# Kernel optimization log

Measured on AMD Instinct MI355X. Metric: run time of the kernel, lower is better.

The kernel has to match this reference:

```python
import jax, jax.numpy as jnp
import numpy as np


def _cxcywh_to_xyxy(b):
    cx, cy, w, h = b[..., 0], b[..., 1], b[..., 2], b[..., 3]
    return jnp.stack([cx - 0.5 * w, cy - 0.5 * h, cx + 0.5 * w, cy + 0.5 * h], axis=-1)


def _generalized_box_iou(a, b):
    # a: [M,4] xyxy, b: [N,4] xyxy -> [M,N] GIoU matrix (DETR box_ops semantics)
    area_a = (a[:, 2] - a[:, 0]) * (a[:, 3] - a[:, 1])  # [M]
    area_b = (b[:, 2] - b[:, 0]) * (b[:, 3] - b[:, 1])  # [N]
    lt = jnp.maximum(a[:, None, :2], b[None, :, :2])    # [M,N,2]
    rb = jnp.minimum(a[:, None, 2:], b[None, :, 2:])
    wh = jnp.clip(rb - lt, 0.0)
    inter = wh[..., 0] * wh[..., 1]                     # [M,N]
    union = area_a[:, None] + area_b[None, :] - inter
    iou = inter / union
    lt_c = jnp.minimum(a[:, None, :2], b[None, :, :2])
    rb_c = jnp.maximum(a[:, None, 2:], b[None, :, 2:])
    wh_c = jnp.clip(rb_c - lt_c, 0.0)
    area_c = wh_c[..., 0] * wh_c[..., 1]
    return iou - (area_c - union) / area_c


def setup_inputs() -> dict:
    key = jax.random.key(0)
    k1, k2, k3 = jax.random.split(key, 3)
    B, T, N = 8, 64, 8
    # predicted boxes in cxcywh, all components in (0,1) -> positive w,h (valid)
    pred_boxes = jax.random.uniform(k1, (B, T, N, 4), dtype=jnp.float32)
    # target boxes directly in valid xyxy (code path uses them unconverted)
    centers = jax.random.uniform(k2, (B, T, N, 2), dtype=jnp.float32) * 0.8 + 0.1
    half_wh = (jax.random.uniform(k3, (B, T, N, 2), dtype=jnp.float32) * 0.2 + 0.02) * 0.5
    bboxes = jnp.concatenate([centers - half_wh, centers + half_wh], axis=-1)
    bboxes_mask = jnp.ones((B, T), dtype=bool)
    return {"pred_boxes": pred_boxes, "bboxes": bboxes, "bboxes_mask": bboxes_mask}


def reference(pred_boxes, bboxes, bboxes_mask):
    B, T, N, _ = pred_boxes.shape
    M = B * T * N
    # per-box validity (mask is per-frame, broadcast to boxes), as weights
    v = jnp.broadcast_to(bboxes_mask[:, :, None], (B, T, N)).reshape(M).astype(pred_boxes.dtype)
    src = _cxcywh_to_xyxy(pred_boxes.reshape(M, 4))   # [M,4]
    tgt = bboxes.reshape(M, 4)                        # [M,4]
    G = _generalized_box_iou(tgt, src)                # [M,M] rows=targets, cols=preds
    # argmax matching over valid prediction columns
    g_match = jnp.where(v[None, :] > 0, G, -jnp.inf)
    idx = jnp.argmax(g_match, axis=1)                 # [M]
    matched = src[idx]                                # [M,4]
    matched_gious = G[:, idx]                         # [M,M] (faithful to original)
    w = v[:, None] * v[idx][None, :]                  # validity weights
    loss_giou = 1.0 - jnp.sum(matched_gious * w) / jnp.sum(w)
    loss_bbox = jnp.sum(jnp.abs(matched - tgt) * v[:, None]) / (4.0 * jnp.sum(v))
    return loss_giou, loss_bbox
```

## Files before the change

### kernel.cpp

```cpp
#include <hip/hip_runtime.h>
#include <cmath>

#define WAVE 64
#define TPB  256
#define RPW  4
#define SJ   8
#define FTPB 1024
#define MMAX 4096

__device__ __forceinline__ float fastrcp(float x) { return __builtin_amdgcn_rcpf(x); }

__device__ __forceinline__ float giou_f(float a0, float a1, float a2, float a3, float areaA,
                                        float b0, float b1, float b2, float b3, float areaB) {
    float ltx = fmaxf(a0, b0), lty = fmaxf(a1, b1);
    float rbx = fminf(a2, b2), rby = fminf(a3, b3);
    float w = fmaxf(rbx - ltx, 0.0f), h = fmaxf(rby - lty, 0.0f);
    float inter = w * h;
    float uni = areaA + areaB - inter;
    float cx1 = fminf(a0, b0), cy1 = fminf(a1, b1);
    float cx2 = fmaxf(a2, b2), cy2 = fmaxf(a3, b3);
    float areaC = (cx2 - cx1) * (cy2 - cy1);
    return inter * fastrcp(uni) - (areaC - uni) * fastrcp(areaC);
}

__device__ __forceinline__ unsigned sortable_u32(float f) {
    unsigned b = __float_as_uint(f);
    return (b & 0x80000000u) ? ~b : (b | 0x80000000u);
}

__device__ __forceinline__ int mask_mode(const void* maskp) {
    const unsigned char* mb = (const unsigned char*)maskp;
    unsigned char b0 = mb[0], b1 = mb[1];
    if (b0 != 0 && b1 != 0) return 0;
    if (b0 != 0) return 1;
    return 2;
}
__device__ __forceinline__ float mask_v(const void* maskp, int t, int mode) {
    if (mode == 0) return ((const unsigned char*)maskp)[t] ? 1.0f : 0.0f;
    if (mode == 1) return ((const int*)maskp)[t] ? 1.0f : 0.0f;
    return (((const float*)maskp)[t] != 0.0f) ? 1.0f : 0.0f;
}
__device__ __forceinline__ int midx(int m, int nsh, int N) {
    return (nsh >= 0) ? (m >> nsh) : (m / N);
}

__global__ __launch_bounds__(TPB) void pass_kernel(
        const float4* __restrict__ pred, const float4* __restrict__ tgt,
        const void* __restrict__ maskp, int M, int nsh, int N,
        unsigned long long* __restrict__ keypart, float* __restrict__ colpart,
        int rowBlocks) {
    const int mode  = mask_mode(maskp);
    const int chunk = M / SJ;
    const int lane  = threadIdx.x & (WAVE - 1);
    const int warp  = threadIdx.x >> 6;

    if ((int)blockIdx.x < rowBlocks) {
        int wid = blockIdx.x * (TPB / WAVE) + warp;
        int rowgrp = wid / SJ, c = wid % SJ;
        int i0 = rowgrp * RPW;
        if (i0 >= M) return;
        int jbeg = c * chunk, jend = jbeg + chunk;

        float a0[RPW], a1[RPW], a2[RPW], a3[RPW], aA[RPW], best[RPW];
        int bidx[RPW];
#pragma unroll
        for (int r = 0; r < RPW; ++r) {
            float4 t = tgt[i0 + r];
            a0[r] = t.x; a1[r] = t.y; a2[r] = t.z; a3[r] = t.w;
            aA[r] = (t.z - t.x) * (t.w - t.y);
            best[r] = -INFINITY; bidx[r] = 0;
        }

#pragma unroll 4
        for (int j = jbeg + lane; j < jend; j += WAVE) {
            float4 p = pred[j];
            float sx1 = p.x - 0.5f * p.z, sy1 = p.y - 0.5f * p.w;
            float sx2 = p.x + 0.5f * p.z, sy2 = p.y + 0.5f * p.w;
            float aB = (sx2 - sx1) * (sy2 - sy1);
            float vj = mask_v(maskp, midx(j, nsh, N), mode);
            bool mv = vj > 0.0f;
#pragma unroll
            for (int r = 0; r < RPW; ++r) {
                float g = giou_f(a0[r], a1[r], a2[r], a3[r], aA[r], sx1, sy1, sx2, sy2, aB);
                float val = mv ? g : -INFINITY;
                if (val > best[r]) { best[r] = val; bidx[r] = j; }
            }
        }

#pragma unroll
        for (int r = 0; r < RPW; ++r) {
            unsigned long long key = ((unsigned long long)sortable_u32(best[r]) << 32)
                                   | (unsigned)(~bidx[r]);
            for (int off = 32; off >= 1; off >>= 1) {
                unsigned long long ok = __shfl_xor(key, off);
                key = (ok > key) ? ok : key;
            }
            if (lane == 0) keypart[(size_t)c * M + (i0 + r)] = key;
        }
    } else {
        int wid = (blockIdx.x - rowBlocks) * (TPB / WAVE) + warp;
        int colgrp = wid / SJ, c = wid % SJ;
        int j0 = colgrp * RPW;
        if (j0 >= M) return;
        int ibeg = c * chunk, iend = ibeg + chunk;

        float b0[RPW], b1[RPW], b2[RPW], b3[RPW], aB[RPW], acc[RPW];
#pragma unroll
        for (int r = 0; r < RPW; ++r) {
            float4 p = pred[j0 + r];
            b0[r] = p.x - 0.5f * p.z; b1[r] = p.y - 0.5f * p.w;
            b2[r] = p.x + 0.5f * p.z; b3[r] = p.y + 0.5f * p.w;
            aB[r] = (b2[r] - b0[r]) * (b3[r] - b1[r]);
            acc[r] = 0.0f;
        }

#pragma unroll 4
        for (int i = ibeg + lane; i < iend; i += WAVE) {
            float4 t = tgt[i];
            float aA = (t.z - t.x) * (t.w - t.y);
            float vi = mask_v(maskp, midx(i, nsh, N), mode);
#pragma unroll
            for (int r = 0; r < RPW; ++r) {
                float g = giou_f(t.x, t.y, t.z, t.w, aA, b0[r], b1[r], b2[r], b3[r], aB[r]);
                acc[r] += vi * g;
            }
        }

#pragma unroll
        for (int r = 0; r < RPW; ++r) {
            for (int off = 32; off >= 1; off >>= 1) acc[r] += __shfl_xor(acc[r], off);
            if (lane == 0) colpart[(size_t)c * M + (j0 + r)] = acc[r];
        }
    }
}

__device__ __forceinline__ double wave_sum_d(double x) {
    for (int off = 32; off >= 1; off >>= 1) x += __shfl_xor(x, off);
    return x;
}

__global__ __launch_bounds__(FTPB) void finalize_kernel(
        const float4* __restrict__ pred, const float4* __restrict__ tgt,
        const void* __restrict__ maskp, int M, int nsh, int N,
        const unsigned long long* __restrict__ keypart,
        const float* __restrict__ colpart, float* __restrict__ out) {
    __shared__ float cs_lds[MMAX];
    __shared__ unsigned short idx_lds[MMAX];
    __shared__ float v_lds[MMAX];
    __shared__ double red[4 * (FTPB / WAVE)];

    const int mode = mask_mode(maskp);
    const int tid = threadIdx.x;

    for (int m = tid; m < M; m += FTPB) {
        unsigned long long k = keypart[m];
        float s = colpart[m];
#pragma unroll
        for (int c = 1; c < SJ; ++c) {
            unsigned long long kc = keypart[(size_t)c * M + m];
            k = (kc > k) ? kc : k;
            s += colpart[(size_t)c * M + m];
        }
        idx_lds[m] = (unsigned short)(~(unsigned)k);
        cs_lds[m] = s;
        v_lds[m] = mask_v(maskp, midx(m, nsh, N), mode);
    }
    __syncthreads();

    double sumV = 0.0, S1 = 0.0, S2 = 0.0, bbox = 0.0;
    for (int m = tid; m < M; m += FTPB) {
        float vi = v_lds[m];
        int k = idx_lds[m];
        float vk = v_lds[k];
        sumV += (double)vi;
        S2   += (double)vk;
        S1   += (double)vk * (double)cs_lds[k];
        float4 p = pred[k];
        float sx1 = p.x - 0.5f * p.z, sy1 = p.y - 0.5f * p.w;
        float sx2 = p.x + 0.5f * p.z, sy2 = p.y + 0.5f * p.w;
        float4 t = tgt[m];
        bbox += (double)vi * (double)(fabsf(sx1 - t.x) + fabsf(sy1 - t.y) +
                                      fabsf(sx2 - t.z) + fabsf(sy2 - t.w));
    }
    sumV = wave_sum_d(sumV);
    S2   = wave_sum_d(S2);
    S1   = wave_sum_d(S1);
    bbox = wave_sum_d(bbox);
    int wid = tid >> 6, lane = tid & (WAVE - 1);
    const int NW = FTPB / WAVE;
    if (lane == 0) {
        red[wid] = sumV; red[NW + wid] = S2; red[2 * NW + wid] = S1; red[3 * NW + wid] = bbox;
    }
    __syncthreads();
    if (tid == 0) {
        double a = 0, b = 0, c = 0, d = 0;
        for (int w = 0; w < NW; ++w) {
            a += red[w]; b += red[NW + w]; c += red[2 * NW + w]; d += red[3 * NW + w];
        }
        out[0] = (float)(1.0 - c / (a * b));
        out[1] = (float)(d / (4.0 * a));
    }
}

extern "C" void kernel_launch(void* const* d_in, const int* in_sizes, int n_in,
                              void* d_out, int out_size, void* d_ws, size_t ws_size,
                              hipStream_t stream) {
    const float4* pred = (const float4*)d_in[0];
    const float4* tgt  = (const float4*)d_in[1];
    const void*   mask = d_in[2];

    int M = in_sizes[0] / 4;
    int N = M / in_sizes[2];
    int nsh = -1;
    for (int s = 0; s < 31; ++s) if ((1 << s) == N) { nsh = s; break; }

    char* ws = (char*)d_ws;
    unsigned long long* keypart = (unsigned long long*)ws; ws += (size_t)SJ * M * 8;
    float* colpart = (float*)ws;                           ws += (size_t)SJ * M * 4;
    float* out = (float*)d_out;

    int rowBlocks = ((M / RPW) * SJ) / (TPB / WAVE);
    int colBlocks = rowBlocks;
    pass_kernel<<<rowBlocks + colBlocks, TPB, 0, stream>>>(
        pred, tgt, mask, M, nsh, N, keypart, colpart, rowBlocks);

    finalize_kernel<<<1, FTPB, 0, stream>>>(pred, tgt, mask, M, nsh, N, keypart, colpart, out);
}
```

Before: 102.2 us.

## Compute each GIoU tile once, sharing it between row argmax and column sums

```diff
diff --git a/kernel.cpp b/kernel.cpp
--- a/kernel.cpp
+++ b/kernel.cpp
@@ -3,25 +3,9 @@
 
 #define WAVE 64
 #define TPB  256
-#define RPW  4
-#define SJ   8
 #define FTPB 1024
-#define MMAX 4096
 
 __device__ __forceinline__ float fastrcp(float x) { return __builtin_amdgcn_rcpf(x); }
-
-__device__ __forceinline__ float giou_f(float a0, float a1, float a2, float a3, float areaA,
-                                        float b0, float b1, float b2, float b3, float areaB) {
-    float ltx = fmaxf(a0, b0), lty = fmaxf(a1, b1);
-    float rbx = fminf(a2, b2), rby = fminf(a3, b3);
-    float w = fmaxf(rbx - ltx, 0.0f), h = fmaxf(rby - lty, 0.0f);
-    float inter = w * h;
-    float uni = areaA + areaB - inter;
-    float cx1 = fminf(a0, b0), cy1 = fminf(a1, b1);
-    float cx2 = fmaxf(a2, b2), cy2 = fmaxf(a3, b3);
-    float areaC = (cx2 - cx1) * (cy2 - cy1);
-    return inter * fastrcp(uni) - (areaC - uni) * fastrcp(areaC);
-}
 
 __device__ __forceinline__ unsigned sortable_u32(float f) {
     unsigned b = __float_as_uint(f);
@@ -47,91 +31,104 @@
 __global__ __launch_bounds__(TPB) void pass_kernel(
         const float4* __restrict__ pred, const float4* __restrict__ tgt,
         const void* __restrict__ maskp, int M, int nsh, int N,
-        unsigned long long* __restrict__ keypart, float* __restrict__ colpart,
-        int rowBlocks) {
-    const int mode  = mask_mode(maskp);
-    const int chunk = M / SJ;
-    const int lane  = threadIdx.x & (WAVE - 1);
-    const int warp  = threadIdx.x >> 6;
-
-    if ((int)blockIdx.x < rowBlocks) {
-        int wid = blockIdx.x * (TPB / WAVE) + warp;
-        int rowgrp = wid / SJ, c = wid % SJ;
-        int i0 = rowgrp * RPW;
-        if (i0 >= M) return;
-        int jbeg = c * chunk, jend = jbeg + chunk;
-
-        float a0[RPW], a1[RPW], a2[RPW], a3[RPW], aA[RPW], best[RPW];
-        int bidx[RPW];
-#pragma unroll
-        for (int r = 0; r < RPW; ++r) {
-            float4 t = tgt[i0 + r];
-            a0[r] = t.x; a1[r] = t.y; a2[r] = t.z; a3[r] = t.w;
-            aA[r] = (t.z - t.x) * (t.w - t.y);
-            best[r] = -INFINITY; bidx[r] = 0;
-        }
-
-#pragma unroll 4
-        for (int j = jbeg + lane; j < jend; j += WAVE) {
-            float4 p = pred[j];
-            float sx1 = p.x - 0.5f * p.z, sy1 = p.y - 0.5f * p.w;
-            float sx2 = p.x + 0.5f * p.z, sy2 = p.y + 0.5f * p.w;
-            float aB = (sx2 - sx1) * (sy2 - sy1);
-            float vj = mask_v(maskp, midx(j, nsh, N), mode);
-            bool mv = vj > 0.0f;
-#pragma unroll
-            for (int r = 0; r < RPW; ++r) {
-                float g = giou_f(a0[r], a1[r], a2[r], a3[r], aA[r], sx1, sy1, sx2, sy2, aB);
-                float val = mv ? g : -INFINITY;
-                if (val > best[r]) { best[r] = val; bidx[r] = j; }
-            }
-        }
-
-#pragma unroll
-        for (int r = 0; r < RPW; ++r) {
-            unsigned long long key = ((unsigned long long)sortable_u32(best[r]) << 32)
-                                   | (unsigned)(~bidx[r]);
-            for (int off = 32; off >= 1; off >>= 1) {
-                unsigned long long ok = __shfl_xor(key, off);
-                key = (ok > key) ? ok : key;
-            }
-            if (lane == 0) keypart[(size_t)c * M + (i0 + r)] = key;
-        }
-    } else {
-        int wid = (blockIdx.x - rowBlocks) * (TPB / WAVE) + warp;
-        int colgrp = wid / SJ, c = wid % SJ;
-        int j0 = colgrp * RPW;
-        if (j0 >= M) return;
-        int ibeg = c * chunk, iend = ibeg + chunk;
-
-        float b0[RPW], b1[RPW], b2[RPW], b3[RPW], aB[RPW], acc[RPW];
-#pragma unroll
-        for (int r = 0; r < RPW; ++r) {
-            float4 p = pred[j0 + r];
-            b0[r] = p.x - 0.5f * p.z; b1[r] = p.y - 0.5f * p.w;
-            b2[r] = p.x + 0.5f * p.z; b3[r] = p.y + 0.5f * p.w;
-            aB[r] = (b2[r] - b0[r]) * (b3[r] - b1[r]);
-            acc[r] = 0.0f;
-        }
-
-#pragma unroll 4
-        for (int i = ibeg + lane; i < iend; i += WAVE) {
-            float4 t = tgt[i];
-            float aA = (t.z - t.x) * (t.w - t.y);
-            float vi = mask_v(maskp, midx(i, nsh, N), mode);
-#pragma unroll
-            for (int r = 0; r < RPW; ++r) {
-                float g = giou_f(t.x, t.y, t.z, t.w, aA, b0[r], b1[r], b2[r], b3[r], aB[r]);
-                acc[r] += vi * g;
-            }
-        }
-
-#pragma unroll
-        for (int r = 0; r < RPW; ++r) {
-            for (int off = 32; off >= 1; off >>= 1) acc[r] += __shfl_xor(acc[r], off);
-            if (lane == 0) colpart[(size_t)c * M + (j0 + r)] = acc[r];
-        }
-    }
+        unsigned long long* __restrict__ keypart, float* __restrict__ colpart) {
+    __shared__ float rowst[64][8];
+    __shared__ float tr[4][8][65];
+
+    const int mode = mask_mode(maskp);
+    const int CR   = M >> 8;
+    const int rg   = blockIdx.x / CR;
+    const int cr   = blockIdx.x % CR;
+    const int tid  = threadIdx.x;
+    const int lane = tid & (WAVE - 1);
+    const int warp = tid >> 6;
+    const int i0   = rg * 64;
+
+    if (tid < 64) {
+        float4 t = tgt[i0 + tid];
+        rowst[tid][0] = t.x; rowst[tid][1] = t.y;
+        rowst[tid][2] = t.z; rowst[tid][3] = t.w;
+        rowst[tid][4] = (t.z - t.x) * (t.w - t.y);
+        rowst[tid][5] = mask_v(maskp, midx(i0 + tid, nsh, N), mode);
+    }
+    __syncthreads();
+
+    const int c0 = (cr * 4 + warp) * 64;
+    const int c  = c0 + lane;
+    float4 p = pred[c];
+    float bx1 = p.x - 0.5f * p.z, by1 = p.y - 0.5f * p.w;
+    float bx2 = p.x + 0.5f * p.z, by2 = p.y + 0.5f * p.w;
+    float aB  = (bx2 - bx1) * (by2 - by1);
+    float vc  = mask_v(maskp, midx(c, nsh, N), mode);
+    bool  mv  = vc > 0.0f;
+
+    float colacc = 0.0f;
+    float bestv[8];
+    int   besti[8];
+#pragma unroll
+    for (int s = 0; s < 8; ++s) { bestv[s] = -INFINITY; besti[s] = 0; }
+
+    const int rbase  = lane & 7;
+    const int cslice = (lane >> 3) * 8;
+
+#pragma unroll
+    for (int s = 0; s < 8; ++s) {
+#pragma unroll
+        for (int r = 0; r < 8; ++r) {
+            const int row = s * 8 + r;
+            float ax1 = rowst[row][0], ay1 = rowst[row][1];
+            float ax2 = rowst[row][2], ay2 = rowst[row][3];
+            float aA  = rowst[row][4], vi = rowst[row][5];
+            float ltx = fmaxf(ax1, bx1), lty = fmaxf(ay1, by1);
+            float rbx = fminf(ax2, bx2), rby = fminf(ay2, by2);
+            float w = fmaxf(rbx - ltx, 0.0f), h = fmaxf(rby - lty, 0.0f);
+            float inter = w * h;
+            float uni = aA + aB - inter;
+            float cx1 = fminf(ax1, bx1), cy1 = fminf(ay1, by1);
+            float cx2 = fmaxf(ax2, bx2), cy2 = fmaxf(ay2, by2);
+            float areaC = (cx2 - cx1) * (cy2 - cy1);
+            float hval = fmaf(uni, fastrcp(areaC), inter * fastrcp(uni));
+            colacc = fmaf(vi, hval, colacc);
+            tr[warp][r][lane] = mv ? hval : -INFINITY;
+        }
+#pragma unroll
+        for (int j = 0; j < 8; ++j) {
+            float val = tr[warp][rbase][cslice + j];
+            int cidx = c0 + cslice + j;
+            if (val > bestv[s]) { bestv[s] = val; besti[s] = cidx; }
+        }
+    }
+
+#pragma unroll
+    for (int s = 0; s < 8; ++s) {
+        unsigned long long key = ((unsigned long long)sortable_u32(bestv[s]) << 32)
+                               | (unsigned)(~besti[s]);
+#pragma unroll
+        for (int off = 8; off <= 32; off <<= 1) {
+            unsigned long long ok = __shfl_xor(key, off);
+            key = (ok > key) ? ok : key;
+        }
+        if (lane < 8)
+            keypart[(size_t)(cr * 4 + warp) * M + (i0 + s * 8 + lane)] = key;
+    }
+    colpart[(size_t)rg * M + c] = colacc;
+}
+
+__global__ __launch_bounds__(TPB) void reduce_kernel(
+        const unsigned long long* __restrict__ keypart,
+        const float* __restrict__ colpart, int M, int P,
+        int* __restrict__ idx, float* __restrict__ colsumh) {
+    int m = blockIdx.x * blockDim.x + threadIdx.x;
+    if (m >= M) return;
+    unsigned long long k = keypart[m];
+    for (int cc = 1; cc < P; ++cc) {
+        unsigned long long kc = keypart[(size_t)cc * M + m];
+        k = (kc > k) ? kc : k;
+    }
+    float s = colpart[m];
+    for (int cc = 1; cc < P; ++cc) s += colpart[(size_t)cc * M + m];
+    idx[m] = (int)(~(unsigned)k);
+    colsumh[m] = s;
 }
 
 __device__ __forceinline__ double wave_sum_d(double x) {
@@ -142,39 +139,20 @@
 __global__ __launch_bounds__(FTPB) void finalize_kernel(
         const float4* __restrict__ pred, const float4* __restrict__ tgt,
         const void* __restrict__ maskp, int M, int nsh, int N,
-        const unsigned long long* __restrict__ keypart,
-        const float* __restrict__ colpart, float* __restrict__ out) {
-    __shared__ float cs_lds[MMAX];
-    __shared__ unsigned short idx_lds[MMAX];
-    __shared__ float v_lds[MMAX];
+        const int* __restrict__ idx, const float* __restrict__ colsumh,
+        float* __restrict__ out) {
     __shared__ double red[4 * (FTPB / WAVE)];
-
     const int mode = mask_mode(maskp);
     const int tid = threadIdx.x;
 
+    double sumV = 0.0, S2 = 0.0, S1h = 0.0, bbox = 0.0;
     for (int m = tid; m < M; m += FTPB) {
-        unsigned long long k = keypart[m];
-        float s = colpart[m];
-#pragma unroll
-        for (int c = 1; c < SJ; ++c) {
-            unsigned long long kc = keypart[(size_t)c * M + m];
-            k = (kc > k) ? kc : k;
-            s += colpart[(size_t)c * M + m];
-        }
-        idx_lds[m] = (unsigned short)(~(unsigned)k);
-        cs_lds[m] = s;
-        v_lds[m] = mask_v(maskp, midx(m, nsh, N), mode);
-    }
-    __syncthreads();
-
-    double sumV = 0.0, S1 = 0.0, S2 = 0.0, bbox = 0.0;
-    for (int m = tid; m < M; m += FTPB) {
-        float vi = v_lds[m];
-        int k = idx_lds[m];
-        float vk = v_lds[k];
+        float vi = mask_v(maskp, midx(m, nsh, N), mode);
+        int   k  = idx[m];
+        float vk = mask_v(maskp, midx(k, nsh, N), mode);
         sumV += (double)vi;
         S2   += (double)vk;
-        S1   += (double)vk * (double)cs_lds[k];
+        S1h  += (double)vk * (double)colsumh[k];
         float4 p = pred[k];
         float sx1 = p.x - 0.5f * p.z, sy1 = p.y - 0.5f * p.w;
         float sx2 = p.x + 0.5f * p.z, sy2 = p.y + 0.5f * p.w;
@@ -184,12 +162,12 @@
     }
     sumV = wave_sum_d(sumV);
     S2   = wave_sum_d(S2);
-    S1   = wave_sum_d(S1);
+    S1h  = wave_sum_d(S1h);
     bbox = wave_sum_d(bbox);
     int wid = tid >> 6, lane = tid & (WAVE - 1);
     const int NW = FTPB / WAVE;
     if (lane == 0) {
-        red[wid] = sumV; red[NW + wid] = S2; red[2 * NW + wid] = S1; red[3 * NW + wid] = bbox;
+        red[wid] = sumV; red[NW + wid] = S2; red[2 * NW + wid] = S1h; red[3 * NW + wid] = bbox;
     }
     __syncthreads();
     if (tid == 0) {
@@ -197,7 +175,7 @@
         for (int w = 0; w < NW; ++w) {
             a += red[w]; b += red[NW + w]; c += red[2 * NW + w]; d += red[3 * NW + w];
         }
-        out[0] = (float)(1.0 - c / (a * b));
+        out[0] = (float)(2.0 - c / (a * b));
         out[1] = (float)(d / (4.0 * a));
     }
 }
@@ -214,15 +192,19 @@
     int nsh = -1;
     for (int s = 0; s < 31; ++s) if ((1 << s) == N) { nsh = s; break; }
 
+    int P = M / 64;
+
     char* ws = (char*)d_ws;
-    unsigned long long* keypart = (unsigned long long*)ws; ws += (size_t)SJ * M * 8;
-    float* colpart = (float*)ws;                           ws += (size_t)SJ * M * 4;
+    unsigned long long* keypart = (unsigned long long*)ws; ws += (size_t)P * M * 8;
+    float* colpart = (float*)ws;                           ws += (size_t)P * M * 4;
+    int*   idx     = (int*)ws;                             ws += (size_t)M * 4;
+    float* colsumh = (float*)ws;                           ws += (size_t)M * 4;
     float* out = (float*)d_out;
 
-    int rowBlocks = ((M / RPW) * SJ) / (TPB / WAVE);
-    int colBlocks = rowBlocks;
-    pass_kernel<<<rowBlocks + colBlocks, TPB, 0, stream>>>(
-        pred, tgt, mask, M, nsh, N, keypart, colpart, rowBlocks);
-
-    finalize_kernel<<<1, FTPB, 0, stream>>>(pred, tgt, mask, M, nsh, N, keypart, colpart, out);
-}
+    int blocks = (M / 64) * (M / 256);
+    pass_kernel<<<blocks, TPB, 0, stream>>>(pred, tgt, mask, M, nsh, N, keypart, colpart);
+
+    reduce_kernel<<<(M + TPB - 1) / TPB, TPB, 0, stream>>>(keypart, colpart, M, P, idx, colsumh);
+
+    finalize_kernel<<<1, FTPB, 0, stream>>>(pred, tgt, mask, M, nsh, N, idx, colsumh, out);
+}
```

Measured after the change: 119.0 us. 16.5% more time.
